# Kernel tuning notes

Hardware: AMD Instinct MI355X
Metric: run time of the kernel (lower is better)

Reference implementation:

```python
import jax, jax.numpy as jnp
import numpy as np

HEADS = 4
DIM_HEADS = 32


def setup_inputs() -> dict:
    key = jax.random.key(0)
    ks = jax.random.split(key, 6)
    dim = 128
    hidden = HEADS * DIM_HEADS  # 128
    b, h, w = 4, 64, 64
    s = 0.02
    return {
        "x": jax.random.normal(ks[0], (b, dim, h, w), dtype=jnp.float32),
        "wq": jax.random.normal(ks[1], (hidden, dim), dtype=jnp.float32) * s,
        "wk": jax.random.normal(ks[2], (hidden, dim), dtype=jnp.float32) * s,
        "wv": jax.random.normal(ks[3], (hidden, dim), dtype=jnp.float32) * s,
        "wo": jax.random.normal(ks[4], (dim, hidden), dtype=jnp.float32) * s,
        "bo": jnp.zeros((dim,), dtype=jnp.float32),
    }


def reference(x, wq, wk, wv, wo, bo):
    b, c, h, w = x.shape
    n = h * w
    scale = DIM_HEADS ** (-0.5)
    xt = x.reshape(b, c, n)  # [b, c, n]; 1x1 conv == matmul over channel dim
    # project and split heads: [b, heads, dim_heads, n]
    q = jnp.einsum('oc,bcn->bon', wq, xt).reshape(b, HEADS, DIM_HEADS, n)
    k = jnp.einsum('oc,bcn->bon', wk, xt).reshape(b, HEADS, DIM_HEADS, n)
    v = jnp.einsum('oc,bcn->bon', wv, xt).reshape(b, HEADS, DIM_HEADS, n)
    q = q * scale
    sim = jnp.einsum('bhdi,bhdj->bhij', q, k)  # [b, heads, n, n]
    attn = jax.nn.softmax(sim, axis=-1)
    out = jnp.einsum('bhij,bhdj->bhid', attn, v)  # [b, heads, n, dim_heads]
    # permute to [b, heads, dim_heads, n] then merge heads -> channels
    out = out.transpose(0, 1, 3, 2).reshape(b, HEADS * DIM_HEADS, n)
    out = jnp.einsum('oc,bcn->bon', wo, out) + bo[None, :, None]
    return out.reshape(b, -1, h, w)
```

## Files before the change

### kernel.cpp

```cpp
#include <hip/hip_runtime.h>
#include <cstdint>

typedef __bf16 bf16;
typedef __bf16 bf16x2 __attribute__((ext_vector_type(2)));
typedef __bf16 bf16x4 __attribute__((ext_vector_type(4)));
typedef __bf16 bf16x8 __attribute__((ext_vector_type(8)));
typedef float f32x4 __attribute__((ext_vector_type(4)));
typedef float f32x16 __attribute__((ext_vector_type(16)));

#define MFMA16(a, b, c) __builtin_amdgcn_mfma_f32_16x16x32_bf16(a, b, c, 0, 0, 0)
#define MFMA32(a, b, c) __builtin_amdgcn_mfma_f32_32x32x16_bf16(a, b, c, 0, 0, 0)

static constexpr int N = 4096;
static constexpr int CDIM = 128;
static constexpr int NH = 4;
static constexpr int DH = 32;

__device__ __forceinline__ uint32_t pack_bf16_trunc(float a, float b) {
    return __builtin_amdgcn_perm(__builtin_bit_cast(uint32_t, b),
                                 __builtin_bit_cast(uint32_t, a), 0x07060302u);
}

__device__ __forceinline__ bf16 to_bf16_rnd(float f) {
    uint32_t u = __builtin_bit_cast(uint32_t, f);
    return __builtin_bit_cast(bf16, (uint16_t)((u + 0x8000u) >> 16));
}

__global__ __launch_bounds__(256) void cvt_w(const float* __restrict__ wq,
                                             const float* __restrict__ wk,
                                             const float* __restrict__ wv,
                                             const float* __restrict__ wo,
                                             bf16* __restrict__ W) {
    int i = blockIdx.x * 256 + threadIdx.x;
    const float qs = 0.17677669529663687f * 1.4426950408889634f;
    W[i]         = (bf16)(wq[i] * qs);
    W[16384 + i] = to_bf16_rnd(wk[i]);
    W[32768 + i] = to_bf16_rnd(wv[i]);
    W[49152 + i] = to_bf16_rnd(wo[i]);
}

__global__ __launch_bounds__(256) void proj_qkv(const float* __restrict__ x,
                                                const bf16* __restrict__ W,
                                                bf16* __restrict__ Q,
                                                bf16* __restrict__ K,
                                                bf16* __restrict__ V) {
    const int b = blockIdx.y;
    const int wt = blockIdx.z;
    const int n0 = blockIdx.x * 64;
    __shared__ __align__(16) bf16 xT[64][136];
    const int tid = threadIdx.x;
    const float* xb = x + (size_t)b * CDIM * N;
    for (int i = tid; i < 64 * 32; i += 256) {
        int n4 = (i & 15) * 4, cc = i >> 4;
        const float4 v = *(const float4*)&xb[(size_t)cc * N + n0 + n4];
        xT[n4 + 0][cc] = to_bf16_rnd(v.x);
        xT[n4 + 1][cc] = to_bf16_rnd(v.y);
        xT[n4 + 2][cc] = to_bf16_rnd(v.z);
        xT[n4 + 3][cc] = to_bf16_rnd(v.w);
    }
    __syncthreads();

    const int lane = tid & 63, w = tid >> 6;
    const int cr = lane & 15, quad = lane >> 4;

    const bf16* Wm = W + wt * 16384;
    for (int nt = 0; nt < 4; ++nt) {
        bf16x8 bfr[4];
#pragma unroll
        for (int ks = 0; ks < 4; ++ks)
            bfr[ks] = *(const bf16x8*)&xT[nt * 16 + cr][ks * 32 + quad * 8];
#pragma unroll
        for (int ot2 = 0; ot2 < 2; ++ot2) {
            int ot = w * 2 + ot2;
            f32x4 acc = {0.f, 0.f, 0.f, 0.f};
#pragma unroll
            for (int ks = 0; ks < 4; ++ks) {
                bf16x8 afr = *(const bf16x8*)&Wm[(ot * 16 + cr) * 128 + ks * 32 + quad * 8];
                acc = MFMA16(afr, bfr[ks], acc);
            }
            int n = n0 + nt * 16 + cr;
            int o0 = ot * 16 + quad * 4;
            if (wt < 2) {
                bf16* dst = (wt == 0) ? Q : K;
                int h = o0 >> 5, d0 = o0 & 31;
                bf16* p = dst + (((size_t)(b * NH + h) * N + n) * DH + d0);
                *(bf16x2*)p       = (bf16x2){(bf16)acc[0], (bf16)acc[1]};
                *(bf16x2*)(p + 2) = (bf16x2){(bf16)acc[2], (bf16)acc[3]};
            } else {
                int h = o0 >> 5, d0 = o0 & 31;
                int k6 = nt * 16 + cr;
                int r4 = (k6 >> 2) & 3;
                int slotgrp = ((r4 & 1) << 1) | (r4 >> 1);
                int kperm = (k6 & ~15) | (slotgrp * 4 + (k6 & 3));
                bf16* p = V + ((size_t)(b * NH + h) * 64 + blockIdx.x) * 2048 + kperm;
#pragma unroll
                for (int r = 0; r < 4; ++r)
                    p[(d0 + r) * 64] = (bf16)acc[r];
            }
        }
    }
}

__global__ __launch_bounds__(256, 2) void flash(const bf16* __restrict__ Q,
                                                const bf16* __restrict__ K,
                                                const bf16* __restrict__ V,
                                                bf16* __restrict__ O) {
    const int gid = blockIdx.x;
    const int bh = gid & 15;
    const int qblk = gid >> 4;
    const int tid = threadIdx.x;
    const int w = tid >> 6, lane = tid & 63;
    const int l31 = lane & 31, h = lane >> 5;
    const int qg = w >> 1, kh = w & 1;
    const int qbase = qblk * 128 + qg * 64;

    __shared__ __align__(16) bf16 Kl[2][2][64 * 40];
    __shared__ __align__(16) bf16 Vl[2][2][32 * 72];

    const bf16* Qb = Q + (size_t)bh * N * DH;
    const bf16* Kb = K + (size_t)bh * N * DH;
    const bf16* Vt = V + (size_t)bh * 64 * 2048;

    const bf16* ksrc0 = Kb + tid * 8;
    const bf16* ksrc1 = Kb + 65536 + tid * 8;
    const bf16* vsrc0 = Vt + tid * 8;
    const bf16* vsrc1 = Vt + 65536 + tid * 8;
    const int k_dst = (tid >> 2) * 40 + (tid & 3) * 8;
    const int v_dst = (tid >> 3) * 72 + (tid & 7) * 8;

    bf16x8 qf[2][2];
#pragma unroll
    for (int qs = 0; qs < 2; ++qs)
#pragma unroll
        for (int dh = 0; dh < 2; ++dh)
            qf[qs][dh] = *(const bf16x8*)&Qb[(qbase + qs * 32 + l31) * DH + dh * 16 + h * 8];

    bf16x8 ones;
#pragma unroll
    for (int i = 0; i < 8; ++i) ones[i] = (bf16)1.0f;

    f32x16 out[2] = {};
    f32x16 accL[2] = {};

    *(bf16x8*)&Kl[0][0][k_dst] = *(const bf16x8*)ksrc0;
    *(bf16x8*)&Kl[0][1][k_dst] = *(const bf16x8*)ksrc1;
    *(bf16x8*)&Vl[0][0][v_dst] = *(const bf16x8*)vsrc0;
    *(bf16x8*)&Vl[0][1][v_dst] = *(const bf16x8*)vsrc1;
    __syncthreads();

    for (int kt = 0; kt < 32; ++kt) {
        const int cb = kt & 1;
        bf16x8 pk0, pk1, pv0, pv1;
        if (kt < 31) {
            pk0 = *(const bf16x8*)(ksrc0 + (kt + 1) * 2048);
            pk1 = *(const bf16x8*)(ksrc1 + (kt + 1) * 2048);
            pv0 = *(const bf16x8*)(vsrc0 + (kt + 1) * 2048);
            pv1 = *(const bf16x8*)(vsrc1 + (kt + 1) * 2048);
        }
        const bf16* Kc = &Kl[cb][kh][0];
        const bf16* Vc = &Vl[cb][kh][0];

#pragma unroll
        for (int g2 = 0; g2 < 2; ++g2) {
            bf16x8 kf0 = *(const bf16x8*)&Kc[(g2 * 32 + l31) * 40 + h * 8];
            bf16x8 kf1 = *(const bf16x8*)&Kc[(g2 * 32 + l31) * 40 + 16 + h * 8];
            bf16x8 av0 = *(const bf16x8*)&Vc[l31 * 72 + g2 * 32 + h * 8];
            bf16x8 av1 = *(const bf16x8*)&Vc[l31 * 72 + g2 * 32 + 16 + h * 8];
#pragma unroll
            for (int qs = 0; qs < 2; ++qs) {
                f32x16 sc = {};
                sc = MFMA32(kf0, qf[qs][0], sc);
                sc = MFMA32(kf1, qf[qs][1], sc);

                uint32_t c0 = pack_bf16_trunc(__builtin_amdgcn_exp2f(sc[0]),
                                              __builtin_amdgcn_exp2f(sc[1]));
                uint32_t c1 = pack_bf16_trunc(__builtin_amdgcn_exp2f(sc[2]),
                                              __builtin_amdgcn_exp2f(sc[3]));
                uint32_t c2 = pack_bf16_trunc(__builtin_amdgcn_exp2f(sc[4]),
                                              __builtin_amdgcn_exp2f(sc[5]));
                uint32_t c3 = pack_bf16_trunc(__builtin_amdgcn_exp2f(sc[6]),
                                              __builtin_amdgcn_exp2f(sc[7]));
                uint32_t c4 = pack_bf16_trunc(__builtin_amdgcn_exp2f(sc[8]),
                                              __builtin_amdgcn_exp2f(sc[9]));
                uint32_t c5 = pack_bf16_trunc(__builtin_amdgcn_exp2f(sc[10]),
                                              __builtin_amdgcn_exp2f(sc[11]));
                uint32_t c6 = pack_bf16_trunc(__builtin_amdgcn_exp2f(sc[12]),
                                              __builtin_amdgcn_exp2f(sc[13]));
                uint32_t c7 = pack_bf16_trunc(__builtin_amdgcn_exp2f(sc[14]),
                                              __builtin_amdgcn_exp2f(sc[15]));

                bf16x8 pB0, pB1;
                {
                    uint32_t t0[4] = {c0, c1, c2, c3};
                    uint32_t t1[4] = {c4, c5, c6, c7};
                    pB0 = *(bf16x8*)t0;
                    pB1 = *(bf16x8*)t1;
                }

                out[qs]  = MFMA32(av0, pB0, out[qs]);
                out[qs]  = MFMA32(av1, pB1, out[qs]);
                accL[qs] = MFMA32(ones, pB0, accL[qs]);
                accL[qs] = MFMA32(ones, pB1, accL[qs]);
            }
        }

        if (kt < 31) {
            *(bf16x8*)&Kl[1 - cb][0][k_dst] = pk0;
            *(bf16x8*)&Kl[1 - cb][1][k_dst] = pk1;
            *(bf16x8*)&Vl[1 - cb][0][v_dst] = pv0;
            *(bf16x8*)&Vl[1 - cb][1][v_dst] = pv1;
        }
        __syncthreads();
    }

    float* red = (float*)&Kl[0][0][0];
    if (kh == 1) {
#pragma unroll
        for (int qs = 0; qs < 2; ++qs) {
            float* r = red + ((size_t)((qg * 2 + qs) * 64 + lane)) * 20;
            f32x4 t0 = {out[qs][0], out[qs][1], out[qs][2], out[qs][3]};
            f32x4 t1 = {out[qs][4], out[qs][5], out[qs][6], out[qs][7]};
            f32x4 t2 = {out[qs][8], out[qs][9], out[qs][10], out[qs][11]};
            f32x4 t3 = {out[qs][12], out[qs][13], out[qs][14], out[qs][15]};
            *(f32x4*)(r + 0)  = t0;
            *(f32x4*)(r + 4)  = t1;
            *(f32x4*)(r + 8)  = t2;
            *(f32x4*)(r + 12) = t3;
            r[16] = accL[qs][0];
        }
    }
    __syncthreads();
    if (kh == 0) {
        const int b = bh >> 2, hh = bh & 3;
#pragma unroll
        for (int qs = 0; qs < 2; ++qs) {
            const float* r = red + ((size_t)((qg * 2 + qs) * 64 + lane)) * 20;
#pragma unroll
            for (int i = 0; i < 16; ++i) out[qs][i] += r[i];
            float inv = __builtin_amdgcn_rcpf(accL[qs][0] + r[16]);
            bf16* Ob = O + ((size_t)b * N + qbase + qs * 32 + l31) * CDIM + hh * DH;
#pragma unroll
            for (int rg = 0; rg < 4; ++rg) {
                const int d0 = rg * 8 + h * 4;
                bf16x4 v = {(bf16)(out[qs][rg * 4 + 0] * inv), (bf16)(out[qs][rg * 4 + 1] * inv),
                            (bf16)(out[qs][rg * 4 + 2] * inv), (bf16)(out[qs][rg * 4 + 3] * inv)};
                *(bf16x4*)(Ob + d0) = v;
            }
        }
    }
}

__global__ __launch_bounds__(256) void proj_o(const bf16* __restrict__ A,
                                              const bf16* __restrict__ W,
                                              const float* __restrict__ bo,
                                              float* __restrict__ out) {
    const int b = blockIdx.y;
    const int n0 = blockIdx.x * 64;
    __shared__ __align__(16) bf16 aT[64][136];
    const int tid = threadIdx.x;
    const bf16* Ab = A + (size_t)b * N * CDIM;
    for (int i = tid; i < 64 * 16; i += 256) {
        int c8 = (i & 15) * 8, n = i >> 4;
        *(bf16x8*)&aT[n][c8] = *(const bf16x8*)&Ab[(size_t)(n0 + n) * CDIM + c8];
    }
    __syncthreads();

    const int lane = tid & 63, w = tid >> 6;
    const int cr = lane & 15, quad = lane >> 4;
    const bf16* Wm = W + 3 * 16384;
    const int ot = blockIdx.z * 4 + w;

    for (int nt = 0; nt < 4; ++nt) {
        bf16x8 bfr[4];
#pragma unroll
        for (int ks = 0; ks < 4; ++ks)
            bfr[ks] = *(const bf16x8*)&aT[nt * 16 + cr][ks * 32 + quad * 8];
        f32x4 acc = {0.f, 0.f, 0.f, 0.f};
#pragma unroll
        for (int ks = 0; ks < 4; ++ks) {
            bf16x8 afr = *(const bf16x8*)&Wm[(ot * 16 + cr) * 128 + ks * 32 + quad * 8];
            acc = MFMA16(afr, bfr[ks], acc);
        }
        int n = n0 + nt * 16 + cr;
        int o0 = ot * 16 + quad * 4;
#pragma unroll
        for (int r = 0; r < 4; ++r)
            out[((size_t)b * CDIM + o0 + r) * N + n] = acc[r] + bo[o0 + r];
    }
}

extern "C" void kernel_launch(void* const* d_in, const int* in_sizes, int n_in,
                              void* d_out, int out_size, void* d_ws, size_t ws_size,
                              hipStream_t stream) {
    const float* x  = (const float*)d_in[0];
    const float* wq = (const float*)d_in[1];
    const float* wk = (const float*)d_in[2];
    const float* wv = (const float*)d_in[3];
    const float* wo = (const float*)d_in[4];
    const float* bo = (const float*)d_in[5];

    char* ws = (char*)d_ws;
    bf16* Q = (bf16*)(ws);
    bf16* K = (bf16*)(ws + ((size_t)4 << 20));
    bf16* V = (bf16*)(ws + ((size_t)8 << 20));
    bf16* A = (bf16*)(ws + ((size_t)12 << 20));
    bf16* W = (bf16*)(ws + ((size_t)16 << 20));

    cvt_w<<<64, 256, 0, stream>>>(wq, wk, wv, wo, W);
    proj_qkv<<<dim3(64, 4, 3), 256, 0, stream>>>(x, W, Q, K, V);
    flash<<<512, 256, 0, stream>>>(Q, K, V, A);
    proj_o<<<dim3(64, 4, 2), 256, 0, stream>>>(A, W, bo, (float*)d_out);
}
```

Before: 132.4 us.

## Split flash keys four ways across 512-thread blocks with merged row-sum accumulator

The flash kernel grows from 256 to 512 threads, with each block still covering 128 queries. Keys are now split across four wave groups (kh 0..3) that each stream a quarter of the key range, instead of two halves. The double-buffered LDS is replaced by single-buffer staging with register prefetch and two barriers per step. Row sums use masked ones-matrices so a single accL accumulator holds both query sub-tiles, which frees registers. The final reduction combines three partial outputs through LDS. The goal is more waves for latency hiding and a shorter sequential key loop, at the cost of extra barriers and a larger reduction.

```diff
diff --git a/kernel.cpp b/kernel.cpp
--- a/kernel.cpp
+++ b/kernel.cpp
@@ -101,7 +101,7 @@
     }
 }
 
-__global__ __launch_bounds__(256, 2) void flash(const bf16* __restrict__ Q,
+__global__ __launch_bounds__(512, 4) void flash(const bf16* __restrict__ Q,
                                                 const bf16* __restrict__ K,
                                                 const bf16* __restrict__ V,
                                                 bf16* __restrict__ O) {
@@ -111,22 +111,21 @@
     const int tid = threadIdx.x;
     const int w = tid >> 6, lane = tid & 63;
     const int l31 = lane & 31, h = lane >> 5;
-    const int qg = w >> 1, kh = w & 1;
+    const int qg = w & 1, kh = w >> 1;
     const int qbase = qblk * 128 + qg * 64;
 
-    __shared__ __align__(16) bf16 Kl[2][2][64 * 40];
-    __shared__ __align__(16) bf16 Vl[2][2][32 * 72];
+    __shared__ __align__(16) bf16 Kl[4][64 * 40];
+    __shared__ __align__(16) bf16 Vl[4][32 * 72];
 
     const bf16* Qb = Q + (size_t)bh * N * DH;
     const bf16* Kb = K + (size_t)bh * N * DH;
     const bf16* Vt = V + (size_t)bh * 64 * 2048;
 
-    const bf16* ksrc0 = Kb + tid * 8;
-    const bf16* ksrc1 = Kb + 65536 + tid * 8;
-    const bf16* vsrc0 = Vt + tid * 8;
-    const bf16* vsrc1 = Vt + 65536 + tid * 8;
-    const int k_dst = (tid >> 2) * 40 + (tid & 3) * 8;
-    const int v_dst = (tid >> 3) * 72 + (tid & 7) * 8;
+    const int qtr = tid >> 7, t = tid & 127;
+    const bf16* ksrc = Kb + (size_t)(qtr * 16) * 2048 + t * 16;
+    const bf16* vsrc = Vt + (size_t)(qtr * 16) * 2048 + t * 16;
+    bf16* kdst = &Kl[qtr][(t >> 1) * 40 + (t & 1) * 16];
+    bf16* vdst = &Vl[qtr][(t >> 2) * 72 + (t & 3) * 16];
 
     bf16x8 qf[2][2];
 #pragma unroll
@@ -135,30 +134,39 @@
         for (int dh = 0; dh < 2; ++dh)
             qf[qs][dh] = *(const bf16x8*)&Qb[(qbase + qs * 32 + l31) * DH + dh * 16 + h * 8];
 
-    bf16x8 ones;
-#pragma unroll
-    for (int i = 0; i < 8; ++i) ones[i] = (bf16)1.0f;
+    bf16x8 A1, A2;
+    {
+        bf16 one = (bf16)1.0f, zero = (bf16)0.0f;
+        bf16 v1 = (l31 < 8) ? one : zero;
+        bf16 v2 = (l31 >= 8 && l31 < 16) ? one : zero;
+#pragma unroll
+        for (int i = 0; i < 8; ++i) { A1[i] = v1; A2[i] = v2; }
+    }
 
     f32x16 out[2] = {};
-    f32x16 accL[2] = {};
-
-    *(bf16x8*)&Kl[0][0][k_dst] = *(const bf16x8*)ksrc0;
-    *(bf16x8*)&Kl[0][1][k_dst] = *(const bf16x8*)ksrc1;
-    *(bf16x8*)&Vl[0][0][v_dst] = *(const bf16x8*)vsrc0;
-    *(bf16x8*)&Vl[0][1][v_dst] = *(const bf16x8*)vsrc1;
-    __syncthreads();
-
-    for (int kt = 0; kt < 32; ++kt) {
-        const int cb = kt & 1;
-        bf16x8 pk0, pk1, pv0, pv1;
-        if (kt < 31) {
-            pk0 = *(const bf16x8*)(ksrc0 + (kt + 1) * 2048);
-            pk1 = *(const bf16x8*)(ksrc1 + (kt + 1) * 2048);
-            pv0 = *(const bf16x8*)(vsrc0 + (kt + 1) * 2048);
-            pv1 = *(const bf16x8*)(vsrc1 + (kt + 1) * 2048);
-        }
-        const bf16* Kc = &Kl[cb][kh][0];
-        const bf16* Vc = &Vl[cb][kh][0];
+    f32x16 accL = {};
+
+    bf16x8 kr0 = *(const bf16x8*)(ksrc);
+    bf16x8 kr1 = *(const bf16x8*)(ksrc + 8);
+    bf16x8 vr0 = *(const bf16x8*)(vsrc);
+    bf16x8 vr1 = *(const bf16x8*)(vsrc + 8);
+
+    for (int kt = 0; kt < 16; ++kt) {
+        __syncthreads();
+        *(bf16x8*)(kdst)     = kr0;
+        *(bf16x8*)(kdst + 8) = kr1;
+        *(bf16x8*)(vdst)     = vr0;
+        *(bf16x8*)(vdst + 8) = vr1;
+        __syncthreads();
+        if (kt < 15) {
+            const size_t off = (size_t)(kt + 1) * 2048;
+            kr0 = *(const bf16x8*)(ksrc + off);
+            kr1 = *(const bf16x8*)(ksrc + off + 8);
+            vr0 = *(const bf16x8*)(vsrc + off);
+            vr1 = *(const bf16x8*)(vsrc + off + 8);
+        }
+        const bf16* Kc = &Kl[kh][0];
+        const bf16* Vc = &Vl[kh][0];
 
 #pragma unroll
         for (int g2 = 0; g2 < 2; ++g2) {
@@ -197,53 +205,47 @@
                     pB1 = *(bf16x8*)t1;
                 }
 
-                out[qs]  = MFMA32(av0, pB0, out[qs]);
-                out[qs]  = MFMA32(av1, pB1, out[qs]);
-                accL[qs] = MFMA32(ones, pB0, accL[qs]);
-                accL[qs] = MFMA32(ones, pB1, accL[qs]);
-            }
-        }
-
-        if (kt < 31) {
-            *(bf16x8*)&Kl[1 - cb][0][k_dst] = pk0;
-            *(bf16x8*)&Kl[1 - cb][1][k_dst] = pk1;
-            *(bf16x8*)&Vl[1 - cb][0][v_dst] = pv0;
-            *(bf16x8*)&Vl[1 - cb][1][v_dst] = pv1;
-        }
+                out[qs] = MFMA32(av0, pB0, out[qs]);
+                out[qs] = MFMA32(av1, pB1, out[qs]);
+                const bf16x8 Am = qs ? A2 : A1;
+                accL = MFMA32(Am, pB0, accL);
+                accL = MFMA32(Am, pB1, accL);
+            }
+        }
+    }
+
+    float* red = (float*)&Kl[0][0];
+    const int b = bh >> 2, hh = bh & 3;
+#pragma unroll
+    for (int qs = 0; qs < 2; ++qs) {
+        const float myL = qs ? accL[4] : accL[0];
         __syncthreads();
-    }
-
-    float* red = (float*)&Kl[0][0][0];
-    if (kh == 1) {
-#pragma unroll
-        for (int qs = 0; qs < 2; ++qs) {
-            float* r = red + ((size_t)((qg * 2 + qs) * 64 + lane)) * 20;
-            f32x4 t0 = {out[qs][0], out[qs][1], out[qs][2], out[qs][3]};
-            f32x4 t1 = {out[qs][4], out[qs][5], out[qs][6], out[qs][7]};
-            f32x4 t2 = {out[qs][8], out[qs][9], out[qs][10], out[qs][11]};
-            f32x4 t3 = {out[qs][12], out[qs][13], out[qs][14], out[qs][15]};
-            *(f32x4*)(r + 0)  = t0;
-            *(f32x4*)(r + 4)  = t1;
-            *(f32x4*)(r + 8)  = t2;
-            *(f32x4*)(r + 12) = t3;
-            r[16] = accL[qs][0];
-        }
-    }
-    __syncthreads();
-    if (kh == 0) {
-        const int b = bh >> 2, hh = bh & 3;
-#pragma unroll
-        for (int qs = 0; qs < 2; ++qs) {
-            const float* r = red + ((size_t)((qg * 2 + qs) * 64 + lane)) * 20;
-#pragma unroll
-            for (int i = 0; i < 16; ++i) out[qs][i] += r[i];
-            float inv = __builtin_amdgcn_rcpf(accL[qs][0] + r[16]);
+        if (kh > 0) {
+            float* r = red + (((kh - 1) * 2 + qg) * 64 + lane) * 20;
+            *(f32x4*)(r + 0)  = (f32x4){out[qs][0], out[qs][1], out[qs][2], out[qs][3]};
+            *(f32x4*)(r + 4)  = (f32x4){out[qs][4], out[qs][5], out[qs][6], out[qs][7]};
+            *(f32x4*)(r + 8)  = (f32x4){out[qs][8], out[qs][9], out[qs][10], out[qs][11]};
+            *(f32x4*)(r + 12) = (f32x4){out[qs][12], out[qs][13], out[qs][14], out[qs][15]};
+            r[16] = myL;
+        }
+        __syncthreads();
+        if (kh == 0) {
+            f32x16 o = out[qs];
+            float l = myL;
+#pragma unroll
+            for (int j = 0; j < 3; ++j) {
+                const float* r = red + ((j * 2 + qg) * 64 + lane) * 20;
+#pragma unroll
+                for (int i = 0; i < 16; ++i) o[i] += r[i];
+                l += r[16];
+            }
+            float inv = __builtin_amdgcn_rcpf(l);
             bf16* Ob = O + ((size_t)b * N + qbase + qs * 32 + l31) * CDIM + hh * DH;
 #pragma unroll
             for (int rg = 0; rg < 4; ++rg) {
                 const int d0 = rg * 8 + h * 4;
-                bf16x4 v = {(bf16)(out[qs][rg * 4 + 0] * inv), (bf16)(out[qs][rg * 4 + 1] * inv),
-                            (bf16)(out[qs][rg * 4 + 2] * inv), (bf16)(out[qs][rg * 4 + 3] * inv)};
+                bf16x4 v = {(bf16)(o[rg * 4 + 0] * inv), (bf16)(o[rg * 4 + 1] * inv),
+                            (bf16)(o[rg * 4 + 2] * inv), (bf16)(o[rg * 4 + 3] * inv)};
                 *(bf16x4*)(Ob + d0) = v;
             }
         }
@@ -308,6 +310,6 @@
 
     cvt_w<<<64, 256, 0, stream>>>(wq, wk, wv, wo, W);
     proj_qkv<<<dim3(64, 4, 3), 256, 0, stream>>>(x, W, Q, K, V);
-    flash<<<512, 256, 0, stream>>>(Q, K, V, A);
+    flash<<<512, 512, 0, stream>>>(Q, K, V, A);
     proj_o<<<dim3(64, 4, 2), 256, 0, stream>>>(A, W, bo, (float*)d_out);
 }
```

New measurement: 131.8 us. About the same (-0.5%).
